# Kernel optimization log

Hardware: AMD Instinct MI355X
Metric: run time of the kernel (lower is better)

The kernel has to match this reference:

```python
import jax, jax.numpy as jnp
import numpy as np

EMBED_DIM = 400
HEAD_SIZE = 64


def setup_inputs() -> dict:
    key = jax.random.key(0)
    k1, k2, k3, k4 = jax.random.split(key, 4)
    B, T, C = 8, 2048, EMBED_DIM
    x = jax.random.normal(k1, (B, T, C), dtype=jnp.float32)
    # Linear(embed_dim, head_size, bias=False) weights, stored as [C, H] for x @ W
    s = 1.0 / np.sqrt(C)
    Wq = jax.random.uniform(k2, (C, HEAD_SIZE), dtype=jnp.float32, minval=-s, maxval=s)
    Wk = jax.random.uniform(k3, (C, HEAD_SIZE), dtype=jnp.float32, minval=-s, maxval=s)
    Wv = jax.random.uniform(k4, (C, HEAD_SIZE), dtype=jnp.float32, minval=-s, maxval=s)
    return {"x": x, "Wq": Wq, "Wk": Wk, "Wv": Wv}


def reference(x, Wq, Wk, Wv):
    B, T, C = x.shape
    q = x @ Wq  # [B,T,H]
    k = x @ Wk  # [B,T,H]
    v = x @ Wv  # [B,T,H]
    scale = 1.0 / jnp.sqrt(jnp.asarray(q.shape[-1], q.dtype))
    scores = jnp.einsum('bth,bsh->bts', q, k) * scale  # [B,T,T]
    causal = jnp.tril(jnp.ones((T, T), dtype=bool))
    scores = jnp.where(causal, scores, jnp.asarray(-jnp.inf, scores.dtype))
    attn = jax.nn.softmax(scores, axis=-1)
    out = jnp.einsum('bts,bsh->bth', attn, v)  # [B,T,H]
    return out
```

## Files before the change

kernel.cpp:

```cpp
#include <hip/hip_runtime.h>
#include <math.h>

#define B_SZ   8
#define T_SEQ  2048
#define C_DIM  400
#define H_DIM  64
#define NROWS  (B_SZ * T_SEQ)
#define QT_TILES (T_SEQ / 64)
#define LDSTR  424
#define NCH    8
#define TPC    4
#define NKS    13

typedef short s8v  __attribute__((ext_vector_type(8)));
typedef float f32x4 __attribute__((ext_vector_type(4)));
typedef unsigned u32x4 __attribute__((ext_vector_type(4)));

__device__ __forceinline__ unsigned short f2bf(float f) {
    unsigned int u = __float_as_uint(f);
    u = (u + 0x7FFFu + ((u >> 16) & 1u)) >> 16;
    return (unsigned short)u;
}

__device__ __forceinline__ float bf2f(unsigned short u) {
    return __uint_as_float((unsigned)u << 16);
}

__device__ __forceinline__ unsigned cvtpk_bf16(float lo, float hi) {
    unsigned r;
    asm("v_cvt_pk_bf16_f32 %0, %1, %2" : "=v"(r) : "v"(lo), "v"(hi));
    return r;
}

__global__ __launch_bounds__(256) void wprep_kernel(
    const float* __restrict__ Wq, const float* __restrict__ Wk,
    const float* __restrict__ Wv, unsigned short* __restrict__ WtP)
{
    int idx = blockIdx.x * 256 + threadIdx.x;
    int j    = idx & 7;
    int lane = (idx >> 3) & 63;
    int fks  = idx >> 9;
    int f    = fks / NKS;
    int ks   = fks - f * NKS;
    int m    = f >> 2;
    int col  = (f & 3) * 16 + (lane & 15);
    int k    = ks * 32 + (lane >> 4) * 8 + j;
    const float* W = (m == 0) ? Wq : (m == 1) ? Wk : Wv;
    float v = (k < C_DIM) ? W[k * H_DIM + col] : 0.0f;
    if (m == 0) v *= 0.125f * 1.44269504088896f;
    WtP[idx] = f2bf(v);
}

__global__ __launch_bounds__(256) void proj_kernel(
    const float* __restrict__ x, const unsigned short* __restrict__ WtP,
    unsigned short* __restrict__ Qb, unsigned short* __restrict__ Kb,
    unsigned short* __restrict__ Vt)
{
    __shared__ unsigned short xl[32 * LDSTR];
    const int tid = threadIdx.x;
    const int tile = blockIdx.x;

    const float4* __restrict__ x4 = (const float4*)x;
    for (int idx = tid; idx < 32 * 104; idx += 256) {
        int row = idx / 104, c4 = idx - row * 104;
        ushort4 wv;
        if (c4 < 100) {
            float4 v = x4[(size_t)(tile * 32 + row) * 100 + c4];
            wv.x = f2bf(v.x); wv.y = f2bf(v.y); wv.z = f2bf(v.z); wv.w = f2bf(v.w);
        } else { wv.x = wv.y = wv.z = wv.w = 0; }
        *(ushort4*)&xl[row * LDSTR + c4 * 4] = wv;
    }
    __syncthreads();

    const int w = tid >> 6, l = tid & 63;
    const int lr = l & 15, g = l >> 4;

    f32x4 acc[3][2];
#pragma unroll
    for (int fl = 0; fl < 3; ++fl)
#pragma unroll
        for (int rg = 0; rg < 2; ++rg) acc[fl][rg] = (f32x4)0.f;

    const char* const Wp = (const char*)WtP;
    for (int ks = 0; ks < NKS; ++ks) {
        s8v a0 = *(const s8v*)&xl[lr        * LDSTR + ks * 32 + g * 8];
        s8v a1 = *(const s8v*)&xl[(16 + lr) * LDSTR + ks * 32 + g * 8];
#pragma unroll
        for (int fl = 0; fl < 3; ++fl) {
            int f = w * 3 + fl;
            const s8v b = *(const s8v*)(Wp + ((f * NKS + ks) << 10) + (l << 4));
            acc[fl][0] = __builtin_amdgcn_mfma_f32_16x16x32_bf16(a0, b, acc[fl][0], 0, 0, 0);
            acc[fl][1] = __builtin_amdgcn_mfma_f32_16x16x32_bf16(a1, b, acc[fl][1], 0, 0, 0);
        }
    }

#pragma unroll
    for (int fl = 0; fl < 3; ++fl) {
        int f = w * 3 + fl;
        int m = f >> 2, col = (f & 3) * 16 + lr;
#pragma unroll
        for (int rg = 0; rg < 2; ++rg)
#pragma unroll
            for (int r = 0; r < 4; ++r) {
                int row_g = tile * 32 + rg * 16 + g * 4 + r;
                unsigned short bv = f2bf(acc[fl][rg][r]);
                if (m == 0)      Qb[(size_t)row_g * H_DIM + col] = bv;
                else if (m == 1) Kb[(size_t)row_g * H_DIM + col] = bv;
                else {
                    int b = row_g >> 11, t = row_g & 2047;
                    Vt[((size_t)b * H_DIM + col) * T_SEQ + t] = bv;
                }
            }
    }
}

__global__ __launch_bounds__(256) void attn_kernel(
    const unsigned short* __restrict__ Qb, const unsigned short* __restrict__ Kb,
    const unsigned short* __restrict__ Vt,
    unsigned short* __restrict__ Opart, float* __restrict__ lpart)
{
    const int c  = blockIdx.x;
    const int qt = blockIdx.y;
    const int b  = blockIdx.z;
    if (c * TPC > qt) return;
    const int kt0 = c * TPC;
    const int kend = min(kt0 + (TPC - 1), qt);

    __shared__ char smem[2][16384];

    const int tid = threadIdx.x;
    const int w = tid >> 6, l = tid & 63;
    const int lr = l & 15, g = l >> 4;
    const int q0 = qt * 64 + w * 16;

    const int r0 = tid >> 3;
    const int ch = tid & 7;
    const int swz = (ch * 16) ^ ((r0 & 7) << 4);
    const char* const Kg = (const char*)(Kb + (size_t)b * T_SEQ * H_DIM);
    const char* const Vg = (const char*)(Vt + (size_t)b * H_DIM * T_SEQ);

    uint4 kA, kB, vA, vB;
    auto LD = [&](int kt) {
        kA = *(const uint4*)(Kg + (size_t)(kt * 64 + r0     ) * 128 + ch * 16);
        kB = *(const uint4*)(Kg + (size_t)(kt * 64 + r0 + 32) * 128 + ch * 16);
        vA = *(const uint4*)(Vg + (size_t)(r0     ) * 4096 + kt * 128 + ch * 16);
        vB = *(const uint4*)(Vg + (size_t)(r0 + 32) * 4096 + kt * 128 + ch * 16);
    };
    auto ST = [&](int buf) {
        char* Kl = smem[buf];
        char* Vl = smem[buf] + 8192;
        *(uint4*)(Kl + r0 * 128 + swz)        = kA;
        *(uint4*)(Kl + (r0 + 32) * 128 + swz) = kB;
        *(uint4*)(Vl + r0 * 128 + swz)        = vA;
        *(uint4*)(Vl + (r0 + 32) * 128 + swz) = vB;
    };

    s8v aq[2];
#pragma unroll
    for (int s = 0; s < 2; ++s)
        aq[s] = *(const s8v*)&Qb[((size_t)b * T_SEQ + q0 + lr) * H_DIM + s * 32 + g * 8];

    f32x4 acc[4];
#pragma unroll
    for (int f = 0; f < 4; ++f) acc[f] = (f32x4)0.f;
    float lsum = 0.f;

    LD(kt0); ST(0);
    if (kt0 < kend) LD(kt0 + 1);
    __syncthreads();
    int cur = 0;

    for (int kt = kt0; kt <= kend; ++kt) {
        char* const Kl = smem[cur];
        char* const Vl = smem[cur] + 8192;

        f32x4 sacc[4];
#pragma unroll
        for (int f = 0; f < 4; ++f) sacc[f] = (f32x4)0.f;
        __builtin_amdgcn_s_setprio(1);
#pragma unroll
        for (int f = 0; f < 4; ++f)
#pragma unroll
            for (int s = 0; s < 2; ++s) {
                const s8v ak = *(const s8v*)(Kl + (f * 16 + lr) * 128
                                             + (((s * 4 + g) * 16) ^ ((lr & 7) << 4)));
                sacc[f] = __builtin_amdgcn_mfma_f32_16x16x32_bf16(ak, aq[s], sacc[f], 0, 0, 0);
            }
        __builtin_amdgcn_s_setprio(0);

        float p[4][4];
        if (kt == qt) {
            const int q_my = q0 + lr;
#pragma unroll
            for (int f = 0; f < 4; ++f)
#pragma unroll
                for (int r = 0; r < 4; ++r) {
                    float pv = __builtin_amdgcn_exp2f(sacc[f][r]);
                    p[f][r] = ((kt * 64 + f * 16 + g * 4 + r) > q_my) ? 0.0f : pv;
                }
        } else {
#pragma unroll
            for (int f = 0; f < 4; ++f)
#pragma unroll
                for (int r = 0; r < 4; ++r)
                    p[f][r] = __builtin_amdgcn_exp2f(sacc[f][r]);
        }
#pragma unroll
        for (int f = 0; f < 4; ++f)
            lsum += (p[f][0] + p[f][1]) + (p[f][2] + p[f][3]);

        s8v ap[2];
#pragma unroll
        for (int s = 0; s < 2; ++s) {
            unsigned Fa = cvtpk_bf16(p[2 * s][0],     p[2 * s][1]);
            unsigned Fb = cvtpk_bf16(p[2 * s][2],     p[2 * s][3]);
            unsigned Ga = cvtpk_bf16(p[2 * s + 1][0], p[2 * s + 1][1]);
            unsigned Gb = cvtpk_bf16(p[2 * s + 1][2], p[2 * s + 1][3]);
            asm("v_permlane32_swap_b32 %0, %1" : "+v"(Fa), "+v"(Ga));
            asm("v_permlane16_swap_b32 %0, %1" : "+v"(Fa), "+v"(Ga));
            asm("v_permlane32_swap_b32 %0, %1" : "+v"(Fb), "+v"(Gb));
            asm("v_permlane16_swap_b32 %0, %1" : "+v"(Fb), "+v"(Gb));
            u32x4 wv; wv.x = Fa; wv.y = Fb; wv.z = Ga; wv.w = Gb;
            ap[s] = __builtin_bit_cast(s8v, wv);
        }

        __builtin_amdgcn_s_setprio(1);
#pragma unroll
        for (int f = 0; f < 4; ++f)
#pragma unroll
            for (int s = 0; s < 2; ++s) {
                const s8v bv = *(const s8v*)(Vl + (f * 16 + lr) * 128
                                             + (((s * 4 + g) * 16) ^ ((lr & 7) << 4)));
                acc[f] = __builtin_amdgcn_mfma_f32_16x16x32_bf16(ap[s], bv, acc[f], 0, 0, 0);
            }
        __builtin_amdgcn_s_setprio(0);

        if (kt < kend) {
            ST(cur ^ 1);
            if (kt + 1 < kend) LD(kt + 2);
            __syncthreads();
            cur ^= 1;
        }
    }

    lsum += __shfl_xor(lsum, 16, 64);
    lsum += __shfl_xor(lsum, 32, 64);

    const size_t pb = ((size_t)(b * QT_TILES + qt) * NCH + c);
    unsigned short* const Op = Opart + pb * 4096;
#pragma unroll
    for (int f = 0; f < 4; ++f)
#pragma unroll
        for (int r = 0; r < 4; ++r)
            Op[(w * 16 + g * 4 + r) * 64 + f * 16 + lr] = f2bf(acc[f][r]);
    if (l < 16)
        lpart[pb * 64 + w * 16 + l] = lsum;
}

__global__ __launch_bounds__(256) void combine_kernel(
    const unsigned short* __restrict__ Opart, const float* __restrict__ lpart,
    float* __restrict__ out)
{
    const int idx = blockIdx.x * 256 + threadIdx.x;
    const int row = idx >> 4, h4 = idx & 15;
    const int b = row >> 11, t = row & 2047;
    const int qt = t >> 6, r = t & 63;
    const int nch = (qt >> 2) + 1;

    float4 os = make_float4(0.f, 0.f, 0.f, 0.f);
    float ls = 0.f;
    const size_t base = (size_t)(b * QT_TILES + qt) * NCH;
    for (int cc = 0; cc < nch; ++cc) {
        ushort4 v = *(const ushort4*)&Opart[(base + cc) * 4096 + r * 64 + h4 * 4];
        os.x += bf2f(v.x); os.y += bf2f(v.y); os.z += bf2f(v.z); os.w += bf2f(v.w);
        ls += lpart[(base + cc) * 64 + r];
    }
    float inv = 1.0f / ls;
    ((float4*)out)[idx] = make_float4(os.x * inv, os.y * inv, os.z * inv, os.w * inv);
}

extern "C" void kernel_launch(void* const* d_in, const int* in_sizes, int n_in,
                              void* d_out, int out_size, void* d_ws, size_t ws_size,
                              hipStream_t stream)
{
    const float* x  = (const float*)d_in[0];
    const float* Wq = (const float*)d_in[1];
    const float* Wk = (const float*)d_in[2];
    const float* Wv = (const float*)d_in[3];
    float* out = (float*)d_out;

    char* ws = (char*)d_ws;
    unsigned short* WtP = (unsigned short*)(ws);
    unsigned short* Qb = (unsigned short*)(ws + 163840);
    unsigned short* Kb = (unsigned short*)(ws + 163840 + 2097152);
    unsigned short* Vt = (unsigned short*)(ws + 163840 + 2 * 2097152);
    unsigned short* Opart = (unsigned short*)(ws + 163840 + 3 * 2097152);
    float* lpart = (float*)(ws + 163840 + 3 * 2097152 + 16777216);

    wprep_kernel<<<(12 * NKS * 512) / 256, 256, 0, stream>>>(Wq, Wk, Wv, WtP);
    proj_kernel<<<NROWS / 32, 256, 0, stream>>>(x, WtP, Qb, Kb, Vt);
    attn_kernel<<<dim3(NCH, QT_TILES, B_SZ), 256, 0, stream>>>(Qb, Kb, Vt, Opart, lpart);
    combine_kernel<<<(NROWS * H_DIM / 4) / 256, 256, 0, stream>>>(Opart, lpart, out);
}
```

Measured before the change: 43.77 us.

## Double query tile to 128 rows per block and stage K/V via direct global-to-LDS loads

Each attention block now handles 128 query rows, 32 per wave in two 16-row fragments, so every K/V tile staged in LDS feeds twice as many MFMAs. Block count and K/V reload traffic roughly halve. K/V staging switches from register round-trips to global_load_lds async copies issued one tile ahead, with the XOR swizzle applied on the global source address. The partial buffers and the combine kernel are re-indexed for 128-row tiles. The cost is higher register pressure, and the last chunk on the diagonal tile does extra masked work because causal tile granularity is now 128 rows.

```diff
diff --git a/kernel.cpp b/kernel.cpp
--- a/kernel.cpp
+++ b/kernel.cpp
@@ -6,7 +6,7 @@
 #define C_DIM  400
 #define H_DIM  64
 #define NROWS  (B_SZ * T_SEQ)
-#define QT_TILES (T_SEQ / 64)
+#define QT2    (T_SEQ / 128)
 #define LDSTR  424
 #define NCH    8
 #define TPC    4
@@ -30,6 +30,12 @@
     unsigned r;
     asm("v_cvt_pk_bf16_f32 %0, %1, %2" : "=v"(r) : "v"(lo), "v"(hi));
     return r;
+}
+
+__device__ __forceinline__ void gload_lds16(const void* g, void* l) {
+    __builtin_amdgcn_global_load_lds(
+        (const __attribute__((address_space(1))) void*)g,
+        (__attribute__((address_space(3))) void*)l, 16, 0, 0);
 }
 
 __global__ __launch_bounds__(256) void wprep_kernel(
@@ -119,64 +125,67 @@
     const unsigned short* __restrict__ Vt,
     unsigned short* __restrict__ Opart, float* __restrict__ lpart)
 {
-    const int c  = blockIdx.x;
-    const int qt = blockIdx.y;
-    const int b  = blockIdx.z;
-    if (c * TPC > qt) return;
+    const int c = blockIdx.x;
+    const int m = blockIdx.y;
+    const int b = blockIdx.z;
+    if (c * TPC > 2 * m + 1) return;
     const int kt0 = c * TPC;
-    const int kend = min(kt0 + (TPC - 1), qt);
+    const int kend = min(kt0 + (TPC - 1), 2 * m + 1);
 
     __shared__ char smem[2][16384];
 
     const int tid = threadIdx.x;
     const int w = tid >> 6, l = tid & 63;
     const int lr = l & 15, g = l >> 4;
-    const int q0 = qt * 64 + w * 16;
-
-    const int r0 = tid >> 3;
-    const int ch = tid & 7;
-    const int swz = (ch * 16) ^ ((r0 & 7) << 4);
+    const int q0 = m * 128 + w * 32;
+
     const char* const Kg = (const char*)(Kb + (size_t)b * T_SEQ * H_DIM);
     const char* const Vg = (const char*)(Vt + (size_t)b * H_DIM * T_SEQ);
-
-    uint4 kA, kB, vA, vB;
-    auto LD = [&](int kt) {
-        kA = *(const uint4*)(Kg + (size_t)(kt * 64 + r0     ) * 128 + ch * 16);
-        kB = *(const uint4*)(Kg + (size_t)(kt * 64 + r0 + 32) * 128 + ch * 16);
-        vA = *(const uint4*)(Vg + (size_t)(r0     ) * 4096 + kt * 128 + ch * 16);
-        vB = *(const uint4*)(Vg + (size_t)(r0 + 32) * 4096 + kt * 128 + ch * 16);
+    const int rl = l >> 3;
+    const int cs = ((l & 7) ^ rl) * 16;
+
+    auto STAGE = [&](int kt, int buf) {
+        char* const Kl = smem[buf];
+        char* const Vl = smem[buf] + 8192;
+#pragma unroll
+        for (int i = 0; i < 2; ++i) {
+            const int row = w * 16 + i * 8;
+            gload_lds16(Kg + (size_t)(kt * 64 + row + rl) * 128 + cs,
+                        Kl + row * 128);
+            gload_lds16(Vg + (size_t)(row + rl) * 4096 + kt * 128 + cs,
+                        Vl + row * 128);
+        }
     };
-    auto ST = [&](int buf) {
-        char* Kl = smem[buf];
-        char* Vl = smem[buf] + 8192;
-        *(uint4*)(Kl + r0 * 128 + swz)        = kA;
-        *(uint4*)(Kl + (r0 + 32) * 128 + swz) = kB;
-        *(uint4*)(Vl + r0 * 128 + swz)        = vA;
-        *(uint4*)(Vl + (r0 + 32) * 128 + swz) = vB;
-    };
-
-    s8v aq[2];
-#pragma unroll
-    for (int s = 0; s < 2; ++s)
-        aq[s] = *(const s8v*)&Qb[((size_t)b * T_SEQ + q0 + lr) * H_DIM + s * 32 + g * 8];
-
-    f32x4 acc[4];
-#pragma unroll
-    for (int f = 0; f < 4; ++f) acc[f] = (f32x4)0.f;
-    float lsum = 0.f;
-
-    LD(kt0); ST(0);
-    if (kt0 < kend) LD(kt0 + 1);
+
+    s8v aq[2][2];
+#pragma unroll
+    for (int qf = 0; qf < 2; ++qf)
+#pragma unroll
+        for (int s = 0; s < 2; ++s)
+            aq[qf][s] = *(const s8v*)&Qb[((size_t)b * T_SEQ + q0 + qf * 16 + lr) * H_DIM
+                                         + s * 32 + g * 8];
+
+    f32x4 acc[2][4];
+#pragma unroll
+    for (int qf = 0; qf < 2; ++qf)
+#pragma unroll
+        for (int f = 0; f < 4; ++f) acc[qf][f] = (f32x4)0.f;
+    float lsum[2] = {0.f, 0.f};
+
+    STAGE(kt0, 0);
     __syncthreads();
     int cur = 0;
 
     for (int kt = kt0; kt <= kend; ++kt) {
+        if (kt < kend) STAGE(kt + 1, cur ^ 1);
         char* const Kl = smem[cur];
         char* const Vl = smem[cur] + 8192;
 
-        f32x4 sacc[4];
-#pragma unroll
-        for (int f = 0; f < 4; ++f) sacc[f] = (f32x4)0.f;
+        f32x4 sacc[4][2];
+#pragma unroll
+        for (int f = 0; f < 4; ++f)
+#pragma unroll
+            for (int qf = 0; qf < 2; ++qf) sacc[f][qf] = (f32x4)0.f;
         __builtin_amdgcn_s_setprio(1);
 #pragma unroll
         for (int f = 0; f < 4; ++f)
@@ -184,45 +193,51 @@
             for (int s = 0; s < 2; ++s) {
                 const s8v ak = *(const s8v*)(Kl + (f * 16 + lr) * 128
                                              + (((s * 4 + g) * 16) ^ ((lr & 7) << 4)));
-                sacc[f] = __builtin_amdgcn_mfma_f32_16x16x32_bf16(ak, aq[s], sacc[f], 0, 0, 0);
+#pragma unroll
+                for (int qf = 0; qf < 2; ++qf)
+                    sacc[f][qf] = __builtin_amdgcn_mfma_f32_16x16x32_bf16(ak, aq[qf][s], sacc[f][qf], 0, 0, 0);
             }
         __builtin_amdgcn_s_setprio(0);
 
-        float p[4][4];
-        if (kt == qt) {
-            const int q_my = q0 + lr;
+        float p[2][4][4];
+#pragma unroll
+        for (int qf = 0; qf < 2; ++qf)
 #pragma unroll
             for (int f = 0; f < 4; ++f)
 #pragma unroll
-                for (int r = 0; r < 4; ++r) {
-                    float pv = __builtin_amdgcn_exp2f(sacc[f][r]);
-                    p[f][r] = ((kt * 64 + f * 16 + g * 4 + r) > q_my) ? 0.0f : pv;
-                }
-        } else {
+                for (int r = 0; r < 4; ++r)
+                    p[qf][f][r] = __builtin_amdgcn_exp2f(sacc[f][qf][r]);
+#pragma unroll
+        for (int qf = 0; qf < 2; ++qf) {
+            if (kt * 64 + 63 > q0 + qf * 16) {
+                const int q_my = q0 + qf * 16 + lr;
+#pragma unroll
+                for (int f = 0; f < 4; ++f)
+#pragma unroll
+                    for (int r = 0; r < 4; ++r)
+                        if ((kt * 64 + f * 16 + g * 4 + r) > q_my) p[qf][f][r] = 0.0f;
+            }
 #pragma unroll
             for (int f = 0; f < 4; ++f)
-#pragma unroll
-                for (int r = 0; r < 4; ++r)
-                    p[f][r] = __builtin_amdgcn_exp2f(sacc[f][r]);
+                lsum[qf] += (p[qf][f][0] + p[qf][f][1]) + (p[qf][f][2] + p[qf][f][3]);
         }
-#pragma unroll
-        for (int f = 0; f < 4; ++f)
-            lsum += (p[f][0] + p[f][1]) + (p[f][2] + p[f][3]);
-
-        s8v ap[2];
-#pragma unroll
-        for (int s = 0; s < 2; ++s) {
-            unsigned Fa = cvtpk_bf16(p[2 * s][0],     p[2 * s][1]);
-            unsigned Fb = cvtpk_bf16(p[2 * s][2],     p[2 * s][3]);
-            unsigned Ga = cvtpk_bf16(p[2 * s + 1][0], p[2 * s + 1][1]);
-            unsigned Gb = cvtpk_bf16(p[2 * s + 1][2], p[2 * s + 1][3]);
-            asm("v_permlane32_swap_b32 %0, %1" : "+v"(Fa), "+v"(Ga));
-            asm("v_permlane16_swap_b32 %0, %1" : "+v"(Fa), "+v"(Ga));
-            asm("v_permlane32_swap_b32 %0, %1" : "+v"(Fb), "+v"(Gb));
-            asm("v_permlane16_swap_b32 %0, %1" : "+v"(Fb), "+v"(Gb));
-            u32x4 wv; wv.x = Fa; wv.y = Fb; wv.z = Ga; wv.w = Gb;
-            ap[s] = __builtin_bit_cast(s8v, wv);
-        }
+
+        s8v ap[2][2];
+#pragma unroll
+        for (int qf = 0; qf < 2; ++qf)
+#pragma unroll
+            for (int s = 0; s < 2; ++s) {
+                unsigned Fa = cvtpk_bf16(p[qf][2 * s][0],     p[qf][2 * s][1]);
+                unsigned Fb = cvtpk_bf16(p[qf][2 * s][2],     p[qf][2 * s][3]);
+                unsigned Ga = cvtpk_bf16(p[qf][2 * s + 1][0], p[qf][2 * s + 1][1]);
+                unsigned Gb = cvtpk_bf16(p[qf][2 * s + 1][2], p[qf][2 * s + 1][3]);
+                asm("v_permlane32_swap_b32 %0, %1" : "+v"(Fa), "+v"(Ga));
+                asm("v_permlane16_swap_b32 %0, %1" : "+v"(Fa), "+v"(Ga));
+                asm("v_permlane32_swap_b32 %0, %1" : "+v"(Fb), "+v"(Gb));
+                asm("v_permlane16_swap_b32 %0, %1" : "+v"(Fb), "+v"(Gb));
+                u32x4 wv; wv.x = Fa; wv.y = Fb; wv.z = Ga; wv.w = Gb;
+                ap[qf][s] = __builtin_bit_cast(s8v, wv);
+            }
 
         __builtin_amdgcn_s_setprio(1);
 #pragma unroll
@@ -231,30 +246,37 @@
             for (int s = 0; s < 2; ++s) {
                 const s8v bv = *(const s8v*)(Vl + (f * 16 + lr) * 128
                                              + (((s * 4 + g) * 16) ^ ((lr & 7) << 4)));
-                acc[f] = __builtin_amdgcn_mfma_f32_16x16x32_bf16(ap[s], bv, acc[f], 0, 0, 0);
+#pragma unroll
+                for (int qf = 0; qf < 2; ++qf)
+                    acc[qf][f] = __builtin_amdgcn_mfma_f32_16x16x32_bf16(ap[qf][s], bv, acc[qf][f], 0, 0, 0);
             }
         __builtin_amdgcn_s_setprio(0);
 
         if (kt < kend) {
-            ST(cur ^ 1);
-            if (kt + 1 < kend) LD(kt + 2);
             __syncthreads();
             cur ^= 1;
         }
     }
 
-    lsum += __shfl_xor(lsum, 16, 64);
-    lsum += __shfl_xor(lsum, 32, 64);
-
-    const size_t pb = ((size_t)(b * QT_TILES + qt) * NCH + c);
-    unsigned short* const Op = Opart + pb * 4096;
-#pragma unroll
-    for (int f = 0; f < 4; ++f)
-#pragma unroll
-        for (int r = 0; r < 4; ++r)
-            Op[(w * 16 + g * 4 + r) * 64 + f * 16 + lr] = f2bf(acc[f][r]);
-    if (l < 16)
-        lpart[pb * 64 + w * 16 + l] = lsum;
+#pragma unroll
+    for (int qf = 0; qf < 2; ++qf) {
+        lsum[qf] += __shfl_xor(lsum[qf], 16, 64);
+        lsum[qf] += __shfl_xor(lsum[qf], 32, 64);
+    }
+
+    const size_t pb = ((size_t)(b * QT2 + m) * NCH + c);
+    unsigned short* const Op = Opart + pb * 8192;
+#pragma unroll
+    for (int qf = 0; qf < 2; ++qf)
+#pragma unroll
+        for (int f = 0; f < 4; ++f)
+#pragma unroll
+            for (int r = 0; r < 4; ++r)
+                Op[(w * 32 + qf * 16 + g * 4 + r) * 64 + f * 16 + lr] = f2bf(acc[qf][f][r]);
+    if (l < 16) {
+        lpart[pb * 128 + w * 32 + l]      = lsum[0];
+        lpart[pb * 128 + w * 32 + 16 + l] = lsum[1];
+    }
 }
 
 __global__ __launch_bounds__(256) void combine_kernel(
@@ -264,16 +286,16 @@
     const int idx = blockIdx.x * 256 + threadIdx.x;
     const int row = idx >> 4, h4 = idx & 15;
     const int b = row >> 11, t = row & 2047;
-    const int qt = t >> 6, r = t & 63;
-    const int nch = (qt >> 2) + 1;
+    const int m = t >> 7, r = t & 127;
+    const int nch = ((2 * m + 1) >> 2) + 1;
 
     float4 os = make_float4(0.f, 0.f, 0.f, 0.f);
     float ls = 0.f;
-    const size_t base = (size_t)(b * QT_TILES + qt) * NCH;
+    const size_t base = (size_t)(b * QT2 + m) * NCH;
     for (int cc = 0; cc < nch; ++cc) {
-        ushort4 v = *(const ushort4*)&Opart[(base + cc) * 4096 + r * 64 + h4 * 4];
+        ushort4 v = *(const ushort4*)&Opart[(base + cc) * 8192 + r * 64 + h4 * 4];
         os.x += bf2f(v.x); os.y += bf2f(v.y); os.z += bf2f(v.z); os.w += bf2f(v.w);
-        ls += lpart[(base + cc) * 64 + r];
+        ls += lpart[(base + cc) * 128 + r];
     }
     float inv = 1.0f / ls;
     ((float4*)out)[idx] = make_float4(os.x * inv, os.y * inv, os.z * inv, os.w * inv);
@@ -299,6 +321,6 @@
 
     wprep_kernel<<<(12 * NKS * 512) / 256, 256, 0, stream>>>(Wq, Wk, Wv, WtP);
     proj_kernel<<<NROWS / 32, 256, 0, stream>>>(x, WtP, Qb, Kb, Vt);
-    attn_kernel<<<dim3(NCH, QT_TILES, B_SZ), 256, 0, stream>>>(Qb, Kb, Vt, Opart, lpart);
+    attn_kernel<<<dim3(NCH, QT2, B_SZ), 256, 0, stream>>>(Qb, Kb, Vt, Opart, lpart);
     combine_kernel<<<(NROWS * H_DIM / 4) / 256, 256, 0, stream>>>(Opart, lpart, out);
 }
```

New measurement: 44.98 us. 1.03x slower.

## Stage K/V tiles via direct global-to-LDS loads and split keys into finer chunks

Applied to the files above, without the earlier changes.

Replaces register-staged K/V loads (global load into VGPRs then an LDS store) with global_load_lds DMA-style 16-byte loads that write straight into swizzled LDS. Each tile is prefetched at the top of the loop into the alternate buffer. The key-chunk split is halved (2 tiles per chunk, 16 chunks), which raises the attention grid's parallelism. In exchange, the combine kernel must read twice as many partial outputs, and the partial-output workspace doubles.

```diff
diff --git a/kernel.cpp b/kernel.cpp
--- a/kernel.cpp
+++ b/kernel.cpp
@@ -8,8 +8,8 @@
 #define NROWS  (B_SZ * T_SEQ)
 #define QT_TILES (T_SEQ / 64)
 #define LDSTR  424
-#define NCH    8
-#define TPC    4
+#define NCH    16
+#define TPC    2
 #define NKS    13
 
 typedef short s8v  __attribute__((ext_vector_type(8)));
@@ -30,6 +30,12 @@
     unsigned r;
     asm("v_cvt_pk_bf16_f32 %0, %1, %2" : "=v"(r) : "v"(lo), "v"(hi));
     return r;
+}
+
+__device__ __forceinline__ void gload_lds16(const void* g, void* l) {
+    __builtin_amdgcn_global_load_lds(
+        (const __attribute__((address_space(1))) void*)g,
+        (__attribute__((address_space(3))) void*)l, 16, 0, 0);
 }
 
 __global__ __launch_bounds__(256) void wprep_kernel(
@@ -133,26 +139,22 @@
     const int lr = l & 15, g = l >> 4;
     const int q0 = qt * 64 + w * 16;
 
-    const int r0 = tid >> 3;
-    const int ch = tid & 7;
-    const int swz = (ch * 16) ^ ((r0 & 7) << 4);
     const char* const Kg = (const char*)(Kb + (size_t)b * T_SEQ * H_DIM);
     const char* const Vg = (const char*)(Vt + (size_t)b * H_DIM * T_SEQ);
-
-    uint4 kA, kB, vA, vB;
-    auto LD = [&](int kt) {
-        kA = *(const uint4*)(Kg + (size_t)(kt * 64 + r0     ) * 128 + ch * 16);
-        kB = *(const uint4*)(Kg + (size_t)(kt * 64 + r0 + 32) * 128 + ch * 16);
-        vA = *(const uint4*)(Vg + (size_t)(r0     ) * 4096 + kt * 128 + ch * 16);
-        vB = *(const uint4*)(Vg + (size_t)(r0 + 32) * 4096 + kt * 128 + ch * 16);
-    };
-    auto ST = [&](int buf) {
-        char* Kl = smem[buf];
-        char* Vl = smem[buf] + 8192;
-        *(uint4*)(Kl + r0 * 128 + swz)        = kA;
-        *(uint4*)(Kl + (r0 + 32) * 128 + swz) = kB;
-        *(uint4*)(Vl + r0 * 128 + swz)        = vA;
-        *(uint4*)(Vl + (r0 + 32) * 128 + swz) = vB;
+    const int rl = l >> 3;
+    const int cs = ((l & 7) ^ rl) * 16;
+
+    auto STAGE = [&](int kt, int buf) {
+        char* const Kl = smem[buf];
+        char* const Vl = smem[buf] + 8192;
+#pragma unroll
+        for (int i = 0; i < 2; ++i) {
+            const int row = w * 16 + i * 8;
+            gload_lds16(Kg + (size_t)(kt * 64 + row + rl) * 128 + cs,
+                        Kl + row * 128);
+            gload_lds16(Vg + (size_t)(row + rl) * 4096 + kt * 128 + cs,
+                        Vl + row * 128);
+        }
     };
 
     s8v aq[2];
@@ -165,12 +167,12 @@
     for (int f = 0; f < 4; ++f) acc[f] = (f32x4)0.f;
     float lsum = 0.f;
 
-    LD(kt0); ST(0);
-    if (kt0 < kend) LD(kt0 + 1);
+    STAGE(kt0, 0);
     __syncthreads();
     int cur = 0;
 
     for (int kt = kt0; kt <= kend; ++kt) {
+        if (kt < kend) STAGE(kt + 1, cur ^ 1);
         char* const Kl = smem[cur];
         char* const Vl = smem[cur] + 8192;
 
@@ -236,8 +238,6 @@
         __builtin_amdgcn_s_setprio(0);
 
         if (kt < kend) {
-            ST(cur ^ 1);
-            if (kt + 1 < kend) LD(kt + 2);
             __syncthreads();
             cur ^= 1;
         }
@@ -265,7 +265,7 @@
     const int row = idx >> 4, h4 = idx & 15;
     const int b = row >> 11, t = row & 2047;
     const int qt = t >> 6, r = t & 63;
-    const int nch = (qt >> 2) + 1;
+    const int nch = (qt >> 1) + 1;
 
     float4 os = make_float4(0.f, 0.f, 0.f, 0.f);
     float ls = 0.f;
@@ -295,7 +295,7 @@
     unsigned short* Kb = (unsigned short*)(ws + 163840 + 2097152);
     unsigned short* Vt = (unsigned short*)(ws + 163840 + 2 * 2097152);
     unsigned short* Opart = (unsigned short*)(ws + 163840 + 3 * 2097152);
-    float* lpart = (float*)(ws + 163840 + 3 * 2097152 + 16777216);
+    float* lpart = (float*)(ws + 163840 + 3 * 2097152 + 33554432);
 
     wprep_kernel<<<(12 * NKS * 512) / 256, 256, 0, stream>>>(Wq, Wk, Wv, WtP);
     proj_kernel<<<NROWS / 32, 256, 0, stream>>>(x, WtP, Qb, Kb, Vt);
```

New measurement: 48.51 us. 1.11x slower.

## Software-pipeline attention loop so PV of previous tile overlaps next QK^T

Applied to the files above, without the earlier changes.

Restructures the attention inner loop into a skewed pipeline: the P·V MFMAs of tile i-1 are issued right before the QK^T, exp and packing of tile i, so matrix and transcendental/VALU work from adjacent tiles can interleave. The intent is to hide softmax latency behind MFMA work. It adds an extra __syncthreads per iteration, because the V buffer of the previous tile must stay live while the next tile is staged. A bounds guard and rounded-up grid for wprep are also added, but with the current sizes these change nothing.

```diff
diff --git a/kernel.cpp b/kernel.cpp
--- a/kernel.cpp
+++ b/kernel.cpp
@@ -37,6 +37,7 @@
     const float* __restrict__ Wv, unsigned short* __restrict__ WtP)
 {
     int idx = blockIdx.x * 256 + threadIdx.x;
+    if (idx >= 12 * NKS * 512) return;
     int j    = idx & 7;
     int lane = (idx >> 3) & 63;
     int fks  = idx >> 9;
@@ -125,6 +126,7 @@
     if (c * TPC > qt) return;
     const int kt0 = c * TPC;
     const int kend = min(kt0 + (TPC - 1), qt);
+    const int n = kend - kt0 + 1;
 
     __shared__ char smem[2][16384];
 
@@ -164,16 +166,10 @@
 #pragma unroll
     for (int f = 0; f < 4; ++f) acc[f] = (f32x4)0.f;
     float lsum = 0.f;
-
-    LD(kt0); ST(0);
-    if (kt0 < kend) LD(kt0 + 1);
-    __syncthreads();
-    int cur = 0;
-
-    for (int kt = kt0; kt <= kend; ++kt) {
-        char* const Kl = smem[cur];
-        char* const Vl = smem[cur] + 8192;
-
+    s8v ap[2];
+
+    auto QKT_SM = [&](int kt, int buf) {
+        char* const Kl = smem[buf];
         f32x4 sacc[4];
 #pragma unroll
         for (int f = 0; f < 4; ++f) sacc[f] = (f32x4)0.f;
@@ -209,7 +205,6 @@
         for (int f = 0; f < 4; ++f)
             lsum += (p[f][0] + p[f][1]) + (p[f][2] + p[f][3]);
 
-        s8v ap[2];
 #pragma unroll
         for (int s = 0; s < 2; ++s) {
             unsigned Fa = cvtpk_bf16(p[2 * s][0],     p[2 * s][1]);
@@ -223,7 +218,10 @@
             u32x4 wv; wv.x = Fa; wv.y = Fb; wv.z = Ga; wv.w = Gb;
             ap[s] = __builtin_bit_cast(s8v, wv);
         }
-
+    };
+
+    auto PV = [&](int buf) {
+        char* const Vl = smem[buf] + 8192;
         __builtin_amdgcn_s_setprio(1);
 #pragma unroll
         for (int f = 0; f < 4; ++f)
@@ -234,14 +232,29 @@
                 acc[f] = __builtin_amdgcn_mfma_f32_16x16x32_bf16(ap[s], bv, acc[f], 0, 0, 0);
             }
         __builtin_amdgcn_s_setprio(0);
-
-        if (kt < kend) {
-            ST(cur ^ 1);
-            if (kt + 1 < kend) LD(kt + 2);
-            __syncthreads();
-            cur ^= 1;
+    };
+
+    LD(kt0); ST(0);
+    if (n > 1) LD(kt0 + 1);
+    __syncthreads();
+    QKT_SM(kt0, 0);
+    if (n > 1) {
+        ST(1);
+        if (n > 2) LD(kt0 + 2);
+    }
+    __syncthreads();
+
+    for (int ii = 1; ii < n; ++ii) {
+        PV((ii - 1) & 1);
+        QKT_SM(kt0 + ii, ii & 1);
+        __syncthreads();
+        if (ii + 1 < n) {
+            ST((ii + 1) & 1);
+            if (ii + 2 < n) LD(kt0 + ii + 2);
         }
-    }
+        __syncthreads();
+    }
+    PV((n - 1) & 1);
 
     lsum += __shfl_xor(lsum, 16, 64);
     lsum += __shfl_xor(lsum, 32, 64);
@@ -297,7 +310,7 @@
     unsigned short* Opart = (unsigned short*)(ws + 163840 + 3 * 2097152);
     float* lpart = (float*)(ws + 163840 + 3 * 2097152 + 16777216);
 
-    wprep_kernel<<<(12 * NKS * 512) / 256, 256, 0, stream>>>(Wq, Wk, Wv, WtP);
+    wprep_kernel<<<(12 * NKS * 512 + 255) / 256, 256, 0, stream>>>(Wq, Wk, Wv, WtP);
     proj_kernel<<<NROWS / 32, 256, 0, stream>>>(x, WtP, Qb, Kb, Vt);
     attn_kernel<<<dim3(NCH, QT_TILES, B_SZ), 256, 0, stream>>>(Qb, Kb, Vt, Opart, lpart);
     combine_kernel<<<(NROWS * H_DIM / 4) / 256, 256, 0, stream>>>(Opart, lpart, out);
```

Measured after the change: 44.45 us. About the same (+1.6%).
